# Kernel optimization log

Measured on AMD Instinct MI355X. Metric: run time of the kernel, lower is better.

Reference implementation:

```python
import jax, jax.numpy as jnp
import numpy as np

N = 50000        # nodes
E = 800000       # edges
F_IN = 128       # num_node_features
H = 128          # hidden_size
C = 128          # num_classes (must be 128 for lin1 to typecheck)
G = 64           # graphs in batch


def setup_inputs() -> dict:
    key = jax.random.key(0)
    ks = jax.random.split(key, 12)
    x = jax.random.normal(ks[0], (N, F_IN), dtype=jnp.float32)
    edge_index = jax.random.randint(ks[1], (2, E), 0, N, dtype=jnp.int64)
    batch = jnp.sort(jax.random.randint(ks[2], (N,), 0, G, dtype=jnp.int64))

    def glorot(k, i, o):
        return jax.random.normal(k, (i, o), dtype=jnp.float32) / np.float32(np.sqrt(i))

    return {
        'x': x, 'edge_index': edge_index, 'batch': batch,
        'W1': glorot(ks[3], F_IN, H), 'b1': jnp.zeros((H,), jnp.float32),
        'W2': glorot(ks[4], H, H),    'b2': jnp.zeros((H,), jnp.float32),
        'W3': glorot(ks[5], H, C),    'b3': jnp.zeros((C,), jnp.float32),
        'Wl': glorot(ks[6], 128, C),  'bl': jnp.zeros((C,), jnp.float32),
    }


def _gcn_conv(x, W, b, src, dst, n):
    # PyG GCNConv: h = x W; out_i = sum_{j->i} d_j^-1/2 d_i^-1/2 h_j + b
    h = x @ W                                                   # [n, out]
    deg = jax.ops.segment_sum(jnp.ones(dst.shape[0], h.dtype), dst, num_segments=n)
    dinv = jnp.where(deg > 0, jax.lax.rsqrt(jnp.maximum(deg, 1.0)), 0.0)
    norm = dinv[src] * dinv[dst]                                # [E+n]
    msg = h[src] * norm[:, None]                                # gather + scale
    return jax.ops.segment_sum(msg, dst, num_segments=n) + b    # scatter-add


def reference(x, edge_index, batch, W1, b1, W2, b2, W3, b3, Wl, bl):
    x = x.astype(jnp.float32)
    loops = jnp.arange(N, dtype=edge_index.dtype)
    src = jnp.concatenate([edge_index[0], loops])  # add self-loops
    dst = jnp.concatenate([edge_index[1], loops])

    h = jax.nn.elu(_gcn_conv(x, W1, b1, src, dst, N))
    h = jax.nn.elu(_gcn_conv(h, W2, b2, src, dst, N))
    h = jax.nn.elu(_gcn_conv(h, W3, b3, src, dst, N))

    # global_mean_pool over batch vector
    cnt = jax.ops.segment_sum(jnp.ones(N, h.dtype), batch, num_segments=G)
    pooled = jax.ops.segment_sum(h, batch, num_segments=G) / jnp.maximum(cnt, 1.0)[:, None]

    # dropout(p=0.2) is identity in eval mode
    return pooled @ Wl + bl
```

## Files before the change

kernel.cpp:

```cpp
#include <hip/hip_runtime.h>
#include <hip/hip_bf16.h>
#include <hip/hip_fp16.h>

#define N_NODES 50000
#define N_GRAPHS 64
#define POOL_CHUNK 32
#define FILL_CHUNK 4096
#define SLOTS 64
#define SLOT_SHIFT 6
#define PSHIFT 7
#define NPARTS ((N_NODES + 127) >> 7)

typedef _Float16 f16x8 __attribute__((ext_vector_type(8)));
typedef float f32x4 __attribute__((ext_vector_type(4)));


__device__ inline unsigned short f2h_bits(float x) {
    _Float16 h = (_Float16)x;
    return __builtin_bit_cast(unsigned short, h);
}
__device__ inline float h_bits2f(unsigned short b) {
    return (float)__builtin_bit_cast(_Float16, b);
}
__device__ inline unsigned pack_h2(float a, float b) {
    return (unsigned)f2h_bits(a) | ((unsigned)f2h_bits(b) << 16);
}

__device__ inline void fma_h8(float (&acc)[8], uint4 v, float w) {
    acc[0] += w * h_bits2f((unsigned short)(v.x & 0xffffu));
    acc[1] += w * h_bits2f((unsigned short)(v.x >> 16));
    acc[2] += w * h_bits2f((unsigned short)(v.y & 0xffffu));
    acc[3] += w * h_bits2f((unsigned short)(v.y >> 16));
    acc[4] += w * h_bits2f((unsigned short)(v.z & 0xffffu));
    acc[5] += w * h_bits2f((unsigned short)(v.z >> 16));
    acc[6] += w * h_bits2f((unsigned short)(v.w & 0xffffu));
    acc[7] += w * h_bits2f((unsigned short)(v.w >> 16));
}


__global__ __launch_bounds__(256) void prep_kernel(const int* __restrict__ dst,
                                                   int* __restrict__ cntmat,
                                                   const float* __restrict__ W1,
                                                   const float* __restrict__ W2,
                                                   const float* __restrict__ W3,
                                                   unsigned short* __restrict__ Wt,
                                                   float* __restrict__ pooled,
                                                   int ne, int nch) {
    int blk = blockIdx.x;
    if (blk < nch) {
        __shared__ int h[NPARTS];
        for (int i = threadIdx.x; i < NPARTS; i += 256) h[i] = 0;
        __syncthreads();
        int beg = blk * FILL_CHUNK, end = min(beg + FILL_CHUNK, ne);
        for (int i = beg + threadIdx.x; i < end; i += 256)
            atomicAdd(&h[dst[i] >> PSHIFT], 1);
        __syncthreads();
        for (int i = threadIdx.x; i < NPARTS; i += 256) cntmat[blk * NPARTS + i] = h[i];
    } else if (blk < nch + 192) {
        int i = (blk - nch) * 256 + threadIdx.x;
        int which = i >> 14;
        const float* W = (which == 0) ? W1 : (which == 1) ? W2 : W3;
        int j = i & 16383;
        int nn = j >> 7, k = j & 127;
        Wt[(which << 14) + nn * 128 + k] = f2h_bits(W[k * 128 + nn]);
    } else {
        int i = (blk - nch - 192) * 256 + threadIdx.x;
        if (i < N_GRAPHS * 128) pooled[i] = 0.f;
    }
}


__global__ __launch_bounds__(256) void scanp_kernel(int* __restrict__ cntmat,
                                                    int* __restrict__ ptotal, int nchunks) {
    __shared__ int s[256];
    int p = blockIdx.x, t = threadIdx.x;
    int v = (t < nchunks) ? cntmat[t * NPARTS + p] : 0;
    s[t] = v;
    __syncthreads();
    #pragma unroll
    for (int d = 1; d < 256; d <<= 1) {
        int y = (t >= d) ? s[t - d] : 0;
        __syncthreads();
        s[t] += y;
        __syncthreads();
    }
    if (t < nchunks) cntmat[t * NPARTS + p] = s[t] - v;
    if (t == 255) ptotal[p] = s[255];
}

__global__ __launch_bounds__(512) void scant_kernel(const int* __restrict__ ptotal,
                                                    int* __restrict__ pbase) {
    __shared__ int s[512];
    int t = threadIdx.x;
    int v = (t < NPARTS) ? ptotal[t] : 0;
    s[t] = v;
    __syncthreads();
    #pragma unroll
    for (int d = 1; d < 512; d <<= 1) {
        int y = (t >= d) ? s[t - d] : 0;
        __syncthreads();
        s[t] += y;
        __syncthreads();
    }
    if (t < NPARTS) pbase[t] = s[t] - v;
    if (t == NPARTS - 1) pbase[NPARTS] = s[t];
}

__global__ __launch_bounds__(256) void bin_scatter_kernel(const int* __restrict__ src,
                                                          const int* __restrict__ dst,
                                                          const int* __restrict__ cntmat,
                                                          const int* __restrict__ pbase,
                                                          unsigned* __restrict__ binned, int ne) {
    __shared__ int pos[NPARTS];
    int c = blockIdx.x, t = threadIdx.x;
    for (int i = t; i < NPARTS; i += 256) pos[i] = pbase[i] + cntmat[c * NPARTS + i];
    __syncthreads();
    int beg = c * FILL_CHUNK, end = min(beg + FILL_CHUNK, ne);
    for (int i = beg + t; i < end; i += 256) {
        int d = dst[i];
        int p = d >> PSHIFT;
        int idx = atomicAdd(&pos[p], 1);
        binned[idx] = ((unsigned)(d & 127) << 16) | (unsigned)src[i];
    }
}

__global__ __launch_bounds__(256) void bucket_fill_kernel(const unsigned* __restrict__ binned,
                                                          const int* __restrict__ pbase,
                                                          int* __restrict__ deg,
                                                          float* __restrict__ dinv,
                                                          unsigned* __restrict__ tag,
                                                          uint4* __restrict__ cvp4, int n) {
    __shared__ unsigned bkt[128 * SLOTS];
    __shared__ int curls[128];
    int p = blockIdx.x, t = threadIdx.x;
    if (t < 128) curls[t] = 0;
    __syncthreads();
    int beg = pbase[p], end = pbase[p + 1];
    for (int i = beg + t; i < end; i += 256) {
        unsigned e = binned[i];
        int dl = (int)(e >> 16);
        int ps = atomicAdd(&curls[dl], 1);
        if (ps < SLOTS) bkt[(dl << SLOT_SHIFT) + ps] = e & 0xFFFFu;
    }
    __syncthreads();
    int node0 = p << PSHIFT;
    if (t < 128 && node0 + t < n) {
        int c = curls[t];
        deg[node0 + t] = c;
        float dv = rsqrtf((float)c + 1.0f);
        dinv[node0 + t] = dv;
        tag[node0 + t] = ((unsigned)(node0 + t) << 16) | (unsigned)f2h_bits(dv);
    }
    const uint4* b4 = (const uint4*)bkt;
    uint4* outp = cvp4 + (size_t)p * (128 * SLOTS / 4);
    for (int i = t; i < 128 * SLOTS / 4; i += 256) outp[i] = b4[i];
}

__global__ __launch_bounds__(256) void tagify_kernel(const int* __restrict__ deg,
                                                     const unsigned* __restrict__ tag,
                                                     uint4* __restrict__ cvp4, int n) {
    int t = blockIdx.x * 256 + threadIdx.x;
    int node = t >> 4;
    if (node >= n) return;
    int slot0 = (t & 15) << 2;
    int dg = min(deg[node], SLOTS);
    int lim = (dg + 7) & ~7;
    if (slot0 >= lim) return;
    uint4 v = cvp4[t];
    uint4 r;
    r.x = (slot0     < dg) ? tag[v.x & 0xFFFFu] : 0u;
    r.y = (slot0 + 1 < dg) ? tag[v.y & 0xFFFFu] : 0u;
    r.z = (slot0 + 2 < dg) ? tag[v.z & 0xFFFFu] : 0u;
    r.w = (slot0 + 3 < dg) ? tag[v.w & 0xFFFFu] : 0u;
    cvp4[t] = r;
}


template<bool F32IN>
__global__ __launch_bounds__(256) void mfma_matmul_kernel(const void* __restrict__ Ain,
                                                          const unsigned short* __restrict__ Wt,
                                                          unsigned short* __restrict__ Hh,
                                                          int n) {
    __shared__ unsigned short Wl[128 * 136];
    int t = threadIdx.x;
    {
        int row = t >> 1, seg = t & 1;
        #pragma unroll
        for (int j = 0; j < 8; ++j) {
            int c = seg * 64 + j * 8;
            *(uint4*)&Wl[row * 136 + c] = *(const uint4*)&Wt[row * 128 + c];
        }
    }
    __syncthreads();

    int w = t >> 6, lane = t & 63;
    int lm = lane & 15, lg = lane >> 4;
    int r0 = blockIdx.x * 64 + w * 16;

    f32x4 acc[8];
    #pragma unroll
    for (int ct = 0; ct < 8; ++ct) acc[ct] = (f32x4){0.f, 0.f, 0.f, 0.f};

    int ar = min(r0 + lm, n - 1);

    #pragma unroll
    for (int kk = 0; kk < 4; ++kk) {
        f16x8 a;
        if (F32IN) {
            const float* arow = (const float*)Ain + (size_t)ar * 128;
            float4 lo = *(const float4*)&arow[kk * 32 + lg * 8];
            float4 hi = *(const float4*)&arow[kk * 32 + lg * 8 + 4];
            a[0] = (_Float16)lo.x; a[1] = (_Float16)lo.y;
            a[2] = (_Float16)lo.z; a[3] = (_Float16)lo.w;
            a[4] = (_Float16)hi.x; a[5] = (_Float16)hi.y;
            a[6] = (_Float16)hi.z; a[7] = (_Float16)hi.w;
        } else {
            const unsigned short* arow = (const unsigned short*)Ain + (size_t)ar * 128;
            a = *(const f16x8*)&arow[kk * 32 + lg * 8];
        }
        #pragma unroll
        for (int ct = 0; ct < 8; ++ct) {
            f16x8 b = *(const f16x8*)&Wl[(ct * 16 + lm) * 136 + kk * 32 + lg * 8];
            acc[ct] = __builtin_amdgcn_mfma_f32_16x16x32_f16(a, b, acc[ct], 0, 0, 0);
        }
    }

    #pragma unroll
    for (int ct = 0; ct < 8; ++ct) {
        #pragma unroll
        for (int i = 0; i < 4; ++i) {
            int rr = r0 + lg * 4 + i;
            if (rr < n) Hh[(size_t)rr * 128 + ct * 16 + lm] = f2h_bits(acc[ct][i]);
        }
    }
}


__global__ __launch_bounds__(256) void fused_agg_mm_kernel(const uint4* __restrict__ hb4,
                                                           const int* __restrict__ deg,
                                                           const uint4* __restrict__ cvp4,
                                                           const float* __restrict__ dinv,
                                                           const float* __restrict__ bias,
                                                           const unsigned short* __restrict__ Wt,
                                                           unsigned short* __restrict__ Hh,
                                                           int n) {
    __shared__ unsigned short Wl[128 * 136];
    __shared__ unsigned short actl[16 * 136];
    int t = threadIdx.x;

    {
        int row = t >> 1, seg = t & 1;
        #pragma unroll
        for (int j = 0; j < 8; ++j) {
            int c = seg * 64 + j * 8;
            *(uint4*)&Wl[row * 136 + c] = *(const uint4*)&Wt[row * 128 + c];
        }
    }

    int nl = t >> 4;
    int li = t & 15;
    int node = blockIdx.x * 16 + nl;

    int dg = min(deg[node], SLOTS);
    int n8 = (dg + 7) >> 3;
    const uint4* bucket = cvp4 + ((size_t)node << (SLOT_SHIFT - 2));
    float di = dinv[node];

    float acc[8];
    #pragma unroll
    for (int i = 0; i < 8; ++i) acc[i] = 0.f;

    uint4 h = hb4[(size_t)node * 16 + li];
    fma_h8(acc, h, di);

    uint4 c0 = make_uint4(0, 0, 0, 0), c1 = c0;
    if (n8 > 0) { c0 = bucket[0]; c1 = bucket[1]; }
    for (int e8 = 0; e8 < n8; ++e8) {
        uint4 nx0 = make_uint4(0, 0, 0, 0), nx1 = nx0;
        if (e8 + 1 < n8) { nx0 = bucket[2 * e8 + 2]; nx1 = bucket[2 * e8 + 3]; }
        uint4 v0 = hb4[(size_t)(c0.x >> 16) * 16 + li];
        uint4 v1 = hb4[(size_t)(c0.y >> 16) * 16 + li];
        uint4 v2 = hb4[(size_t)(c0.z >> 16) * 16 + li];
        uint4 v3 = hb4[(size_t)(c0.w >> 16) * 16 + li];
        uint4 v4 = hb4[(size_t)(c1.x >> 16) * 16 + li];
        uint4 v5 = hb4[(size_t)(c1.y >> 16) * 16 + li];
        uint4 v6 = hb4[(size_t)(c1.z >> 16) * 16 + li];
        uint4 v7 = hb4[(size_t)(c1.w >> 16) * 16 + li];
        fma_h8(acc, v0, h_bits2f((unsigned short)(c0.x & 0xffffu)));
        fma_h8(acc, v1, h_bits2f((unsigned short)(c0.y & 0xffffu)));
        fma_h8(acc, v2, h_bits2f((unsigned short)(c0.z & 0xffffu)));
        fma_h8(acc, v3, h_bits2f((unsigned short)(c0.w & 0xffffu)));
        fma_h8(acc, v4, h_bits2f((unsigned short)(c1.x & 0xffffu)));
        fma_h8(acc, v5, h_bits2f((unsigned short)(c1.y & 0xffffu)));
        fma_h8(acc, v6, h_bits2f((unsigned short)(c1.z & 0xffffu)));
        fma_h8(acc, v7, h_bits2f((unsigned short)(c1.w & 0xffffu)));
        c0 = nx0; c1 = nx1;
    }

    float4 b0 = *(const float4*)&bias[li * 8];
    float4 b1 = *(const float4*)&bias[li * 8 + 4];
    float o[8];
    o[0] = di * acc[0] + b0.x; o[1] = di * acc[1] + b0.y;
    o[2] = di * acc[2] + b0.z; o[3] = di * acc[3] + b0.w;
    o[4] = di * acc[4] + b1.x; o[5] = di * acc[5] + b1.y;
    o[6] = di * acc[6] + b1.z; o[7] = di * acc[7] + b1.w;
    #pragma unroll
    for (int i = 0; i < 8; ++i) o[i] = o[i] > 0.f ? o[i] : expm1f(o[i]);
    uint4 pk;
    pk.x = pack_h2(o[0], o[1]);
    pk.y = pack_h2(o[2], o[3]);
    pk.z = pack_h2(o[4], o[5]);
    pk.w = pack_h2(o[6], o[7]);
    *(uint4*)&actl[nl * 136 + li * 8] = pk;

    __syncthreads();

    int w = t >> 6, lane = t & 63;
    int lm = lane & 15, lg = lane >> 4;

    f32x4 macc[2];
    macc[0] = (f32x4){0.f, 0.f, 0.f, 0.f};
    macc[1] = (f32x4){0.f, 0.f, 0.f, 0.f};

    #pragma unroll
    for (int kk = 0; kk < 4; ++kk) {
        f16x8 a = *(const f16x8*)&actl[lm * 136 + kk * 32 + lg * 8];
        #pragma unroll
        for (int j = 0; j < 2; ++j) {
            int ct = w * 2 + j;
            f16x8 b = *(const f16x8*)&Wl[(ct * 16 + lm) * 136 + kk * 32 + lg * 8];
            macc[j] = __builtin_amdgcn_mfma_f32_16x16x32_f16(a, b, macc[j], 0, 0, 0);
        }
    }

    #pragma unroll
    for (int j = 0; j < 2; ++j) {
        int ct = w * 2 + j;
        #pragma unroll
        for (int i = 0; i < 4; ++i) {
            int rr = blockIdx.x * 16 + lg * 4 + i;
            Hh[(size_t)rr * 128 + ct * 16 + lm] = f2h_bits(macc[j][i]);
        }
    }
}


__global__ __launch_bounds__(256) void aggregate_kernel(const uint4* __restrict__ hb4,
                                                        const int* __restrict__ deg,
                                                        const uint4* __restrict__ cvp4,
                                                        const float* __restrict__ dinv,
                                                        const float* __restrict__ bias,
                                                        uint4* __restrict__ outh, int n) {
    int node = blockIdx.x * 16 + (threadIdx.x >> 4);
    if (node >= n) return;
    int li = threadIdx.x & 15;

    int dg = min(deg[node], SLOTS);
    int n8 = (dg + 7) >> 3;
    const uint4* bucket = cvp4 + ((size_t)node << (SLOT_SHIFT - 2));
    float di = dinv[node];

    float acc[8];
    #pragma unroll
    for (int i = 0; i < 8; ++i) acc[i] = 0.f;

    uint4 h = hb4[(size_t)node * 16 + li];
    fma_h8(acc, h, di);

    uint4 c0 = make_uint4(0, 0, 0, 0), c1 = c0;
    if (n8 > 0) { c0 = bucket[0]; c1 = bucket[1]; }
    for (int e8 = 0; e8 < n8; ++e8) {
        uint4 nx0 = make_uint4(0, 0, 0, 0), nx1 = nx0;
        if (e8 + 1 < n8) { nx0 = bucket[2 * e8 + 2]; nx1 = bucket[2 * e8 + 3]; }
        uint4 v0 = hb4[(size_t)(c0.x >> 16) * 16 + li];
        uint4 v1 = hb4[(size_t)(c0.y >> 16) * 16 + li];
        uint4 v2 = hb4[(size_t)(c0.z >> 16) * 16 + li];
        uint4 v3 = hb4[(size_t)(c0.w >> 16) * 16 + li];
        uint4 v4 = hb4[(size_t)(c1.x >> 16) * 16 + li];
        uint4 v5 = hb4[(size_t)(c1.y >> 16) * 16 + li];
        uint4 v6 = hb4[(size_t)(c1.z >> 16) * 16 + li];
        uint4 v7 = hb4[(size_t)(c1.w >> 16) * 16 + li];
        fma_h8(acc, v0, h_bits2f((unsigned short)(c0.x & 0xffffu)));
        fma_h8(acc, v1, h_bits2f((unsigned short)(c0.y & 0xffffu)));
        fma_h8(acc, v2, h_bits2f((unsigned short)(c0.z & 0xffffu)));
        fma_h8(acc, v3, h_bits2f((unsigned short)(c0.w & 0xffffu)));
        fma_h8(acc, v4, h_bits2f((unsigned short)(c1.x & 0xffffu)));
        fma_h8(acc, v5, h_bits2f((unsigned short)(c1.y & 0xffffu)));
        fma_h8(acc, v6, h_bits2f((unsigned short)(c1.z & 0xffffu)));
        fma_h8(acc, v7, h_bits2f((unsigned short)(c1.w & 0xffffu)));
        c0 = nx0; c1 = nx1;
    }

    float4 b0 = *(const float4*)&bias[li * 8];
    float4 b1 = *(const float4*)&bias[li * 8 + 4];
    float o[8];
    o[0] = di * acc[0] + b0.x; o[1] = di * acc[1] + b0.y;
    o[2] = di * acc[2] + b0.z; o[3] = di * acc[3] + b0.w;
    o[4] = di * acc[4] + b1.x; o[5] = di * acc[5] + b1.y;
    o[6] = di * acc[6] + b1.z; o[7] = di * acc[7] + b1.w;
    #pragma unroll
    for (int i = 0; i < 8; ++i) o[i] = o[i] > 0.f ? o[i] : expm1f(o[i]);
    uint4 pk;
    pk.x = pack_h2(o[0], o[1]);
    pk.y = pack_h2(o[2], o[3]);
    pk.z = pack_h2(o[4], o[5]);
    pk.w = pack_h2(o[6], o[7]);
    outh[(size_t)node * 16 + li] = pk;
}


__global__ __launch_bounds__(128) void pool_partial_kernel(const unsigned short* __restrict__ acth,
                                                           const int* __restrict__ batch,
                                                           float* __restrict__ pooled, int n) {
    int f = threadIdx.x;
    int start = blockIdx.x * POOL_CHUNK;
    if (start >= n) return;
    int end = min(start + POOL_CHUNK, n);

    float local = 0.f;
    int gprev = batch[start];
    for (int i = start; i < end; ++i) {
        int g = batch[i];
        if (g != gprev) {
            atomicAdd(&pooled[gprev * 128 + f], local);
            local = 0.f;
            gprev = g;
        }
        local += h_bits2f(acth[(size_t)i * 128 + f]);
    }
    atomicAdd(&pooled[gprev * 128 + f], local);
}


__global__ __launch_bounds__(128) void linear_kernel(const float* __restrict__ pooled,
                                                     const int* __restrict__ batch,
                                                     const float* __restrict__ Wl,
                                                     const float* __restrict__ bl,
                                                     float* __restrict__ out, int n) {
    __shared__ float p[128];
    int g = blockIdx.x, t = threadIdx.x;

    int lo = 0, hi = n;
    while (lo < hi) { int m = (lo + hi) >> 1; if (batch[m] < g) lo = m + 1; else hi = m; }
    int s0 = lo;
    hi = n;
    while (lo < hi) { int m = (lo + hi) >> 1; if (batch[m] < g + 1) lo = m + 1; else hi = m; }
    int e0 = lo;
    float cntf = (float)max(e0 - s0, 1);

    p[t] = pooled[g * 128 + t] / cntf;
    __syncthreads();
    float acc = bl[t];
    for (int k = 0; k < 128; ++k) acc += p[k] * Wl[k * 128 + t];
    out[g * 128 + t] = acc;
}


extern "C" void kernel_launch(void* const* d_in, const int* in_sizes, int n_in,
                              void* d_out, int out_size, void* d_ws, size_t ws_size,
                              hipStream_t stream) {
    const float* x     = (const float*)d_in[0];
    const int*   ei    = (const int*)d_in[1];
    const int*   batch = (const int*)d_in[2];
    const float* W1 = (const float*)d_in[3];
    const float* b1 = (const float*)d_in[4];
    const float* W2 = (const float*)d_in[5];
    const float* b2 = (const float*)d_in[6];
    const float* W3 = (const float*)d_in[7];
    const float* b3 = (const float*)d_in[8];
    const float* Wl = (const float*)d_in[9];
    const float* bl = (const float*)d_in[10];
    float* out = (float*)d_out;

    const int N_ = N_NODES;
    const int E_ = in_sizes[1] / 2;
    const int G_ = N_GRAPHS;
    const int* src = ei;
    const int* dst = ei + E_;
    const int NCH = (E_ + FILL_CHUNK - 1) / FILL_CHUNK;

    char* ws = (char*)d_ws;
    size_t off = 0;
    auto alloc = [&](size_t bytes) -> char* {
        char* p = ws + off;
        off += (bytes + 255) & ~(size_t)255;
        return p;
    };

    float*          dinv   = (float*)          alloc((size_t)N_ * 4);
    unsigned*       tag    = (unsigned*)       alloc((size_t)N_ * 4);
    int*            deg    = (int*)            alloc((size_t)N_ * 4);
    int*            cntmat = (int*)            alloc((size_t)NCH * NPARTS * 4);
    int*            ptotal = (int*)            alloc((size_t)NPARTS * 4);
    int*            pbase  = (int*)            alloc((size_t)(NPARTS + 1) * 4);
    unsigned*       binned = (unsigned*)       alloc((size_t)E_ * 4);
    unsigned*       cvp    = (unsigned*)       alloc((size_t)NPARTS * 128 * SLOTS * 4);
    unsigned short* hbuf   = (unsigned short*) alloc((size_t)N_ * 128 * 2);
    unsigned short* hbuf2  = (unsigned short*) alloc((size_t)N_ * 128 * 2);
    unsigned short* acth   = (unsigned short*) alloc((size_t)N_ * 128 * 2);
    unsigned short* wt     = (unsigned short*) alloc(3 * 128 * 128 * 2);
    float*          pooled = (float*)          alloc((size_t)G_ * 128 * 4);
    (void)ws_size;

    prep_kernel<<<NCH + 192 + 32, 256, 0, stream>>>(dst, cntmat, W1, W2, W3, wt, pooled, E_, NCH);
    scanp_kernel<<<NPARTS, 256, 0, stream>>>(cntmat, ptotal, NCH);
    scant_kernel<<<1, 512, 0, stream>>>(ptotal, pbase);
    bin_scatter_kernel<<<NCH, 256, 0, stream>>>(src, dst, cntmat, pbase, binned, E_);
    bucket_fill_kernel<<<NPARTS, 256, 0, stream>>>(binned, pbase, deg, dinv, tag, (uint4*)cvp, N_);
    tagify_kernel<<<(N_ * 16 + 255) / 256, 256, 0, stream>>>(deg, tag, (uint4*)cvp, N_);

    int mmblocks = (N_ + 63) / 64;
    int agblocks = (N_ + 15) / 16;

    mfma_matmul_kernel<true><<<mmblocks, 256, 0, stream>>>(x, wt, hbuf, N_);
    fused_agg_mm_kernel<<<agblocks, 256, 0, stream>>>((const uint4*)hbuf, deg, (const uint4*)cvp,
                                                      dinv, b1, wt + 16384, hbuf2, N_);
    fused_agg_mm_kernel<<<agblocks, 256, 0, stream>>>((const uint4*)hbuf2, deg, (const uint4*)cvp,
                                                      dinv, b2, wt + 32768, hbuf, N_);
    aggregate_kernel<<<agblocks, 256, 0, stream>>>((const uint4*)hbuf, deg, (const uint4*)cvp,
                                                   dinv, b3, (uint4*)acth, N_);

    pool_partial_kernel<<<(N_ + POOL_CHUNK - 1) / POOL_CHUNK, 128, 0, stream>>>(acth, batch, pooled, N_);
    linear_kernel<<<G_, 128, 0, stream>>>(pooled, batch, Wl, bl, out, N_);
}
```

Before: 180.2 us.

## Fuse final aggregation with mean-pool and merge first matmul into scan kernel

The last GCN aggregation now writes its ELU output into shared memory and accumulates per-graph partial sums directly into the pooled buffer with atomics. This removes the fp16 activation buffer round trip and the separate pooling launch. The first-layer x@W1 MFMA matmul is also folded into the partition scan kernel as extra blocks, so it runs in the same launch as the scan and saves another launch. A shared aggregate_node helper replaces the duplicated aggregation code. The pooling step still issues global atomics per block, and the combined kernel reserves the larger matmul shared buffer even for scan blocks.

```diff
diff --git a/kernel.cpp b/kernel.cpp
--- a/kernel.cpp
+++ b/kernel.cpp
@@ -4,12 +4,12 @@
 
 #define N_NODES 50000
 #define N_GRAPHS 64
-#define POOL_CHUNK 32
 #define FILL_CHUNK 4096
 #define SLOTS 64
 #define SLOT_SHIFT 6
 #define PSHIFT 7
 #define NPARTS ((N_NODES + 127) >> 7)
+#define MM_BLOCKS ((N_NODES + 63) / 64)
 
 typedef _Float16 f16x8 __attribute__((ext_vector_type(8)));
 typedef float f32x4 __attribute__((ext_vector_type(4)));
@@ -35,6 +35,58 @@
     acc[5] += w * h_bits2f((unsigned short)(v.z >> 16));
     acc[6] += w * h_bits2f((unsigned short)(v.w & 0xffffu));
     acc[7] += w * h_bits2f((unsigned short)(v.w >> 16));
+}
+
+__device__ inline void aggregate_node(const uint4* __restrict__ hb4,
+                                      const int* __restrict__ deg,
+                                      const uint4* __restrict__ cvp4,
+                                      const float* __restrict__ dinv,
+                                      const float* __restrict__ bias,
+                                      int node, int li, float (&o)[8]) {
+    int dg = min(deg[node], SLOTS);
+    int n8 = (dg + 7) >> 3;
+    const uint4* bucket = cvp4 + ((size_t)node << (SLOT_SHIFT - 2));
+    float di = dinv[node];
+
+    float acc[8];
+    #pragma unroll
+    for (int i = 0; i < 8; ++i) acc[i] = 0.f;
+
+    uint4 h = hb4[(size_t)node * 16 + li];
+    fma_h8(acc, h, di);
+
+    uint4 c0 = make_uint4(0, 0, 0, 0), c1 = c0;
+    if (n8 > 0) { c0 = bucket[0]; c1 = bucket[1]; }
+    for (int e8 = 0; e8 < n8; ++e8) {
+        uint4 nx0 = make_uint4(0, 0, 0, 0), nx1 = nx0;
+        if (e8 + 1 < n8) { nx0 = bucket[2 * e8 + 2]; nx1 = bucket[2 * e8 + 3]; }
+        uint4 v0 = hb4[(size_t)(c0.x >> 16) * 16 + li];
+        uint4 v1 = hb4[(size_t)(c0.y >> 16) * 16 + li];
+        uint4 v2 = hb4[(size_t)(c0.z >> 16) * 16 + li];
+        uint4 v3 = hb4[(size_t)(c0.w >> 16) * 16 + li];
+        uint4 v4 = hb4[(size_t)(c1.x >> 16) * 16 + li];
+        uint4 v5 = hb4[(size_t)(c1.y >> 16) * 16 + li];
+        uint4 v6 = hb4[(size_t)(c1.z >> 16) * 16 + li];
+        uint4 v7 = hb4[(size_t)(c1.w >> 16) * 16 + li];
+        fma_h8(acc, v0, h_bits2f((unsigned short)(c0.x & 0xffffu)));
+        fma_h8(acc, v1, h_bits2f((unsigned short)(c0.y & 0xffffu)));
+        fma_h8(acc, v2, h_bits2f((unsigned short)(c0.z & 0xffffu)));
+        fma_h8(acc, v3, h_bits2f((unsigned short)(c0.w & 0xffffu)));
+        fma_h8(acc, v4, h_bits2f((unsigned short)(c1.x & 0xffffu)));
+        fma_h8(acc, v5, h_bits2f((unsigned short)(c1.y & 0xffffu)));
+        fma_h8(acc, v6, h_bits2f((unsigned short)(c1.z & 0xffffu)));
+        fma_h8(acc, v7, h_bits2f((unsigned short)(c1.w & 0xffffu)));
+        c0 = nx0; c1 = nx1;
+    }
+
+    float4 b0 = *(const float4*)&bias[li * 8];
+    float4 b1 = *(const float4*)&bias[li * 8 + 4];
+    o[0] = di * acc[0] + b0.x; o[1] = di * acc[1] + b0.y;
+    o[2] = di * acc[2] + b0.z; o[3] = di * acc[3] + b0.w;
+    o[4] = di * acc[4] + b1.x; o[5] = di * acc[5] + b1.y;
+    o[6] = di * acc[6] + b1.z; o[7] = di * acc[7] + b1.w;
+    #pragma unroll
+    for (int i = 0; i < 8; ++i) o[i] = o[i] > 0.f ? o[i] : expm1f(o[i]);
 }
 
 
@@ -70,22 +122,78 @@
 }
 
 
-__global__ __launch_bounds__(256) void scanp_kernel(int* __restrict__ cntmat,
-                                                    int* __restrict__ ptotal, int nchunks) {
-    __shared__ int s[256];
-    int p = blockIdx.x, t = threadIdx.x;
-    int v = (t < nchunks) ? cntmat[t * NPARTS + p] : 0;
-    s[t] = v;
-    __syncthreads();
-    #pragma unroll
-    for (int d = 1; d < 256; d <<= 1) {
-        int y = (t >= d) ? s[t - d] : 0;
+__global__ __launch_bounds__(256) void scanp_mm_kernel(int* __restrict__ cntmat,
+                                                       int* __restrict__ ptotal, int nchunks,
+                                                       const float* __restrict__ x,
+                                                       const unsigned short* __restrict__ Wt,
+                                                       unsigned short* __restrict__ Hh, int n) {
+    __shared__ unsigned short Wl[128 * 136];
+    int blk = blockIdx.x;
+    int t = threadIdx.x;
+
+    if (blk < NPARTS) {
+        int* s = (int*)Wl;
+        int p = blk;
+        int v = (t < nchunks) ? cntmat[t * NPARTS + p] : 0;
+        s[t] = v;
         __syncthreads();
-        s[t] += y;
-        __syncthreads();
-    }
-    if (t < nchunks) cntmat[t * NPARTS + p] = s[t] - v;
-    if (t == 255) ptotal[p] = s[255];
+        #pragma unroll
+        for (int d = 1; d < 256; d <<= 1) {
+            int y = (t >= d) ? s[t - d] : 0;
+            __syncthreads();
+            s[t] += y;
+            __syncthreads();
+        }
+        if (t < nchunks) cntmat[t * NPARTS + p] = s[t] - v;
+        if (t == 255) ptotal[p] = s[255];
+        return;
+    }
+
+    {
+        int row = t >> 1, seg = t & 1;
+        #pragma unroll
+        for (int j = 0; j < 8; ++j) {
+            int c = seg * 64 + j * 8;
+            *(uint4*)&Wl[row * 136 + c] = *(const uint4*)&Wt[row * 128 + c];
+        }
+    }
+    __syncthreads();
+
+    int w = t >> 6, lane = t & 63;
+    int lm = lane & 15, lg = lane >> 4;
+    int r0 = (blk - NPARTS) * 64 + w * 16;
+
+    f32x4 acc[8];
+    #pragma unroll
+    for (int ct = 0; ct < 8; ++ct) acc[ct] = (f32x4){0.f, 0.f, 0.f, 0.f};
+
+    int ar = min(r0 + lm, n - 1);
+
+    #pragma unroll
+    for (int kk = 0; kk < 4; ++kk) {
+        const float* arow = x + (size_t)ar * 128;
+        float4 lo = *(const float4*)&arow[kk * 32 + lg * 8];
+        float4 hi = *(const float4*)&arow[kk * 32 + lg * 8 + 4];
+        f16x8 a;
+        a[0] = (_Float16)lo.x; a[1] = (_Float16)lo.y;
+        a[2] = (_Float16)lo.z; a[3] = (_Float16)lo.w;
+        a[4] = (_Float16)hi.x; a[5] = (_Float16)hi.y;
+        a[6] = (_Float16)hi.z; a[7] = (_Float16)hi.w;
+        #pragma unroll
+        for (int ct = 0; ct < 8; ++ct) {
+            f16x8 b = *(const f16x8*)&Wl[(ct * 16 + lm) * 136 + kk * 32 + lg * 8];
+            acc[ct] = __builtin_amdgcn_mfma_f32_16x16x32_f16(a, b, acc[ct], 0, 0, 0);
+        }
+    }
+
+    #pragma unroll
+    for (int ct = 0; ct < 8; ++ct) {
+        #pragma unroll
+        for (int i = 0; i < 4; ++i) {
+            int rr = r0 + lg * 4 + i;
+            if (rr < n) Hh[(size_t)rr * 128 + ct * 16 + lm] = f2h_bits(acc[ct][i]);
+        }
+    }
 }
 
 __global__ __launch_bounds__(512) void scant_kernel(const int* __restrict__ ptotal,
@@ -176,66 +284,6 @@
 }
 
 
-template<bool F32IN>
-__global__ __launch_bounds__(256) void mfma_matmul_kernel(const void* __restrict__ Ain,
-                                                          const unsigned short* __restrict__ Wt,
-                                                          unsigned short* __restrict__ Hh,
-                                                          int n) {
-    __shared__ unsigned short Wl[128 * 136];
-    int t = threadIdx.x;
-    {
-        int row = t >> 1, seg = t & 1;
-        #pragma unroll
-        for (int j = 0; j < 8; ++j) {
-            int c = seg * 64 + j * 8;
-            *(uint4*)&Wl[row * 136 + c] = *(const uint4*)&Wt[row * 128 + c];
-        }
-    }
-    __syncthreads();
-
-    int w = t >> 6, lane = t & 63;
-    int lm = lane & 15, lg = lane >> 4;
-    int r0 = blockIdx.x * 64 + w * 16;
-
-    f32x4 acc[8];
-    #pragma unroll
-    for (int ct = 0; ct < 8; ++ct) acc[ct] = (f32x4){0.f, 0.f, 0.f, 0.f};
-
-    int ar = min(r0 + lm, n - 1);
-
-    #pragma unroll
-    for (int kk = 0; kk < 4; ++kk) {
-        f16x8 a;
-        if (F32IN) {
-            const float* arow = (const float*)Ain + (size_t)ar * 128;
-            float4 lo = *(const float4*)&arow[kk * 32 + lg * 8];
-            float4 hi = *(const float4*)&arow[kk * 32 + lg * 8 + 4];
-            a[0] = (_Float16)lo.x; a[1] = (_Float16)lo.y;
-            a[2] = (_Float16)lo.z; a[3] = (_Float16)lo.w;
-            a[4] = (_Float16)hi.x; a[5] = (_Float16)hi.y;
-            a[6] = (_Float16)hi.z; a[7] = (_Float16)hi.w;
-        } else {
-            const unsigned short* arow = (const unsigned short*)Ain + (size_t)ar * 128;
-            a = *(const f16x8*)&arow[kk * 32 + lg * 8];
-        }
-        #pragma unroll
-        for (int ct = 0; ct < 8; ++ct) {
-            f16x8 b = *(const f16x8*)&Wl[(ct * 16 + lm) * 136 + kk * 32 + lg * 8];
-            acc[ct] = __builtin_amdgcn_mfma_f32_16x16x32_f16(a, b, acc[ct], 0, 0, 0);
-        }
-    }
-
-    #pragma unroll
-    for (int ct = 0; ct < 8; ++ct) {
-        #pragma unroll
-        for (int i = 0; i < 4; ++i) {
-            int rr = r0 + lg * 4 + i;
-            if (rr < n) Hh[(size_t)rr * 128 + ct * 16 + lm] = f2h_bits(acc[ct][i]);
-        }
-    }
-}
-
-
 __global__ __launch_bounds__(256) void fused_agg_mm_kernel(const uint4* __restrict__ hb4,
                                                            const int* __restrict__ deg,
                                                            const uint4* __restrict__ cvp4,
@@ -261,51 +309,9 @@
     int li = t & 15;
     int node = blockIdx.x * 16 + nl;
 
-    int dg = min(deg[node], SLOTS);
-    int n8 = (dg + 7) >> 3;
-    const uint4* bucket = cvp4 + ((size_t)node << (SLOT_SHIFT - 2));
-    float di = dinv[node];
-
-    float acc[8];
-    #pragma unroll
-    for (int i = 0; i < 8; ++i) acc[i] = 0.f;
-
-    uint4 h = hb4[(size_t)node * 16 + li];
-    fma_h8(acc, h, di);
-
-    uint4 c0 = make_uint4(0, 0, 0, 0), c1 = c0;
-    if (n8 > 0) { c0 = bucket[0]; c1 = bucket[1]; }
-    for (int e8 = 0; e8 < n8; ++e8) {
-        uint4 nx0 = make_uint4(0, 0, 0, 0), nx1 = nx0;
-        if (e8 + 1 < n8) { nx0 = bucket[2 * e8 + 2]; nx1 = bucket[2 * e8 + 3]; }
-        uint4 v0 = hb4[(size_t)(c0.x >> 16) * 16 + li];
-        uint4 v1 = hb4[(size_t)(c0.y >> 16) * 16 + li];
-        uint4 v2 = hb4[(size_t)(c0.z >> 16) * 16 + li];
-        uint4 v3 = hb4[(size_t)(c0.w >> 16) * 16 + li];
-        uint4 v4 = hb4[(size_t)(c1.x >> 16) * 16 + li];
-        uint4 v5 = hb4[(size_t)(c1.y >> 16) * 16 + li];
-        uint4 v6 = hb4[(size_t)(c1.z >> 16) * 16 + li];
-        uint4 v7 = hb4[(size_t)(c1.w >> 16) * 16 + li];
-        fma_h8(acc, v0, h_bits2f((unsigned short)(c0.x & 0xffffu)));
-        fma_h8(acc, v1, h_bits2f((unsigned short)(c0.y & 0xffffu)));
-        fma_h8(acc, v2, h_bits2f((unsigned short)(c0.z & 0xffffu)));
-        fma_h8(acc, v3, h_bits2f((unsigned short)(c0.w & 0xffffu)));
-        fma_h8(acc, v4, h_bits2f((unsigned short)(c1.x & 0xffffu)));
-        fma_h8(acc, v5, h_bits2f((unsigned short)(c1.y & 0xffffu)));
-        fma_h8(acc, v6, h_bits2f((unsigned short)(c1.z & 0xffffu)));
-        fma_h8(acc, v7, h_bits2f((unsigned short)(c1.w & 0xffffu)));
-        c0 = nx0; c1 = nx1;
-    }
-
-    float4 b0 = *(const float4*)&bias[li * 8];
-    float4 b1 = *(const float4*)&bias[li * 8 + 4];
     float o[8];
-    o[0] = di * acc[0] + b0.x; o[1] = di * acc[1] + b0.y;
-    o[2] = di * acc[2] + b0.z; o[3] = di * acc[3] + b0.w;
-    o[4] = di * acc[4] + b1.x; o[5] = di * acc[5] + b1.y;
-    o[6] = di * acc[6] + b1.z; o[7] = di * acc[7] + b1.w;
-    #pragma unroll
-    for (int i = 0; i < 8; ++i) o[i] = o[i] > 0.f ? o[i] : expm1f(o[i]);
+    aggregate_node(hb4, deg, cvp4, dinv, bias, node, li, o);
+
     uint4 pk;
     pk.x = pack_h2(o[0], o[1]);
     pk.y = pack_h2(o[2], o[3]);
@@ -345,88 +351,44 @@
 }
 
 
-__global__ __launch_bounds__(256) void aggregate_kernel(const uint4* __restrict__ hb4,
-                                                        const int* __restrict__ deg,
-                                                        const uint4* __restrict__ cvp4,
-                                                        const float* __restrict__ dinv,
-                                                        const float* __restrict__ bias,
-                                                        uint4* __restrict__ outh, int n) {
-    int node = blockIdx.x * 16 + (threadIdx.x >> 4);
-    if (node >= n) return;
-    int li = threadIdx.x & 15;
-
-    int dg = min(deg[node], SLOTS);
-    int n8 = (dg + 7) >> 3;
-    const uint4* bucket = cvp4 + ((size_t)node << (SLOT_SHIFT - 2));
-    float di = dinv[node];
-
-    float acc[8];
-    #pragma unroll
-    for (int i = 0; i < 8; ++i) acc[i] = 0.f;
-
-    uint4 h = hb4[(size_t)node * 16 + li];
-    fma_h8(acc, h, di);
-
-    uint4 c0 = make_uint4(0, 0, 0, 0), c1 = c0;
-    if (n8 > 0) { c0 = bucket[0]; c1 = bucket[1]; }
-    for (int e8 = 0; e8 < n8; ++e8) {
-        uint4 nx0 = make_uint4(0, 0, 0, 0), nx1 = nx0;
-        if (e8 + 1 < n8) { nx0 = bucket[2 * e8 + 2]; nx1 = bucket[2 * e8 + 3]; }
-        uint4 v0 = hb4[(size_t)(c0.x >> 16) * 16 + li];
-        uint4 v1 = hb4[(size_t)(c0.y >> 16) * 16 + li];
-        uint4 v2 = hb4[(size_t)(c0.z >> 16) * 16 + li];
-        uint4 v3 = hb4[(size_t)(c0.w >> 16) * 16 + li];
-        uint4 v4 = hb4[(size_t)(c1.x >> 16) * 16 + li];
-        uint4 v5 = hb4[(size_t)(c1.y >> 16) * 16 + li];
-        uint4 v6 = hb4[(size_t)(c1.z >> 16) * 16 + li];
-        uint4 v7 = hb4[(size_t)(c1.w >> 16) * 16 + li];
-        fma_h8(acc, v0, h_bits2f((unsigned short)(c0.x & 0xffffu)));
-        fma_h8(acc, v1, h_bits2f((unsigned short)(c0.y & 0xffffu)));
-        fma_h8(acc, v2, h_bits2f((unsigned short)(c0.z & 0xffffu)));
-        fma_h8(acc, v3, h_bits2f((unsigned short)(c0.w & 0xffffu)));
-        fma_h8(acc, v4, h_bits2f((unsigned short)(c1.x & 0xffffu)));
-        fma_h8(acc, v5, h_bits2f((unsigned short)(c1.y & 0xffffu)));
-        fma_h8(acc, v6, h_bits2f((unsigned short)(c1.z & 0xffffu)));
-        fma_h8(acc, v7, h_bits2f((unsigned short)(c1.w & 0xffffu)));
-        c0 = nx0; c1 = nx1;
-    }
-
-    float4 b0 = *(const float4*)&bias[li * 8];
-    float4 b1 = *(const float4*)&bias[li * 8 + 4];
+__global__ __launch_bounds__(256) void fused_agg_pool_kernel(const uint4* __restrict__ hb4,
+                                                             const int* __restrict__ deg,
+                                                             const uint4* __restrict__ cvp4,
+                                                             const float* __restrict__ dinv,
+                                                             const float* __restrict__ bias,
+                                                             const int* __restrict__ batch,
+                                                             float* __restrict__ pooled,
+                                                             int n) {
+    __shared__ float plds[16][132];
+    __shared__ int gid[16];
+    int t = threadIdx.x;
+    int nl = t >> 4;
+    int li = t & 15;
+    int node = blockIdx.x * 16 + nl;
+
+    if (t < 16) gid[t] = batch[blockIdx.x * 16 + t];
+
     float o[8];
-    o[0] = di * acc[0] + b0.x; o[1] = di * acc[1] + b0.y;
-    o[2] = di * acc[2] + b0.z; o[3] = di * acc[3] + b0.w;
-    o[4] = di * acc[4] + b1.x; o[5] = di * acc[5] + b1.y;
-    o[6] = di * acc[6] + b1.z; o[7] = di * acc[7] + b1.w;
-    #pragma unroll
-    for (int i = 0; i < 8; ++i) o[i] = o[i] > 0.f ? o[i] : expm1f(o[i]);
-    uint4 pk;
-    pk.x = pack_h2(o[0], o[1]);
-    pk.y = pack_h2(o[2], o[3]);
-    pk.z = pack_h2(o[4], o[5]);
-    pk.w = pack_h2(o[6], o[7]);
-    outh[(size_t)node * 16 + li] = pk;
-}
-
-
-__global__ __launch_bounds__(128) void pool_partial_kernel(const unsigned short* __restrict__ acth,
-                                                           const int* __restrict__ batch,
-                                                           float* __restrict__ pooled, int n) {
-    int f = threadIdx.x;
-    int start = blockIdx.x * POOL_CHUNK;
-    if (start >= n) return;
-    int end = min(start + POOL_CHUNK, n);
-
+    aggregate_node(hb4, deg, cvp4, dinv, bias, node, li, o);
+
+    #pragma unroll
+    for (int i = 0; i < 8; ++i) plds[nl][li * 8 + i] = o[i];
+
+    __syncthreads();
+
+    int f = t & 127, rg = t >> 7;
+    int r0 = rg * 8;
     float local = 0.f;
-    int gprev = batch[start];
-    for (int i = start; i < end; ++i) {
-        int g = batch[i];
+    int gprev = gid[r0];
+    #pragma unroll
+    for (int r = r0; r < r0 + 8; ++r) {
+        int g = gid[r];
         if (g != gprev) {
             atomicAdd(&pooled[gprev * 128 + f], local);
             local = 0.f;
             gprev = g;
         }
-        local += h_bits2f(acth[(size_t)i * 128 + f]);
+        local += plds[r][f];
     }
     atomicAdd(&pooled[gprev * 128 + f], local);
 }
@@ -497,29 +459,25 @@
     unsigned*       cvp    = (unsigned*)       alloc((size_t)NPARTS * 128 * SLOTS * 4);
     unsigned short* hbuf   = (unsigned short*) alloc((size_t)N_ * 128 * 2);
     unsigned short* hbuf2  = (unsigned short*) alloc((size_t)N_ * 128 * 2);
-    unsigned short* acth   = (unsigned short*) alloc((size_t)N_ * 128 * 2);
     unsigned short* wt     = (unsigned short*) alloc(3 * 128 * 128 * 2);
     float*          pooled = (float*)          alloc((size_t)G_ * 128 * 4);
     (void)ws_size;
 
+    int agblocks = (N_ + 15) / 16;
+
     prep_kernel<<<NCH + 192 + 32, 256, 0, stream>>>(dst, cntmat, W1, W2, W3, wt, pooled, E_, NCH);
-    scanp_kernel<<<NPARTS, 256, 0, stream>>>(cntmat, ptotal, NCH);
+    scanp_mm_kernel<<<NPARTS + MM_BLOCKS, 256, 0, stream>>>(cntmat, ptotal, NCH, x, wt, hbuf, N_);
     scant_kernel<<<1, 512, 0, stream>>>(ptotal, pbase);
     bin_scatter_kernel<<<NCH, 256, 0, stream>>>(src, dst, cntmat, pbase, binned, E_);
     bucket_fill_kernel<<<NPARTS, 256, 0, stream>>>(binned, pbase, deg, dinv, tag, (uint4*)cvp, N_);
     tagify_kernel<<<(N_ * 16 + 255) / 256, 256, 0, stream>>>(deg, tag, (uint4*)cvp, N_);
 
-    int mmblocks = (N_ + 63) / 64;
-    int agblocks = (N_ + 15) / 16;
-
-    mfma_matmul_kernel<true><<<mmblocks, 256, 0, stream>>>(x, wt, hbuf, N_);
     fused_agg_mm_kernel<<<agblocks, 256, 0, stream>>>((const uint4*)hbuf, deg, (const uint4*)cvp,
                                                       dinv, b1, wt + 16384, hbuf2, N_);
     fused_agg_mm_kernel<<<agblocks, 256, 0, stream>>>((const uint4*)hbuf2, deg, (const uint4*)cvp,
                                                       dinv, b2, wt + 32768, hbuf, N_);
-    aggregate_kernel<<<agblocks, 256, 0, stream>>>((const uint4*)hbuf, deg, (const uint4*)cvp,
-                                                   dinv, b3, (uint4*)acth, N_);
-
-    pool_partial_kernel<<<(N_ + POOL_CHUNK - 1) / POOL_CHUNK, 128, 0, stream>>>(acth, batch, pooled, N_);
+    fused_agg_pool_kernel<<<agblocks, 256, 0, stream>>>((const uint4*)hbuf, deg, (const uint4*)cvp,
+                                                        dinv, b3, batch, pooled, N_);
+
     linear_kernel<<<G_, 128, 0, stream>>>(pooled, batch, Wl, bl, out, N_);
 }
```

New measurement: 168.2 us. 1.07x faster.
